# Optimization experiments

Hardware: AMD Instinct MI355X
Metric: run time of the kernel (lower is better)

The kernel has to match this reference:

```python
import jax, jax.numpy as jnp
import numpy as np

N, E, DIM, H = 50000, 800000, 256, 4
HD = DIM // H  # per-head dim = 64
NEG_SLOPE = 0.2
EPS = 1e-5


def _layernorm(x, g, b):
    mu = jnp.mean(x, axis=-1, keepdims=True)
    var = jnp.mean(jnp.square(x - mu), axis=-1, keepdims=True)
    return (x - mu) * jax.lax.rsqrt(var + EPS) * g + b


def setup_inputs() -> dict:
    key = jax.random.key(0)
    ks = jax.random.split(key, 8)
    s = 1.0 / np.sqrt(DIM)
    return {
        "x": jax.random.normal(ks[0], (N, DIM), dtype=jnp.float32),
        "edge_index": jax.random.randint(ks[1], (2, E), 0, N, dtype=jnp.int64),
        "W": jax.random.normal(ks[2], (DIM, DIM), dtype=jnp.float32) * s,
        "a_src": jax.random.normal(ks[3], (H, HD), dtype=jnp.float32) * s,
        "a_dst": jax.random.normal(ks[4], (H, HD), dtype=jnp.float32) * s,
        "gat_b": jnp.zeros((DIM,), jnp.float32),
        "ln1_g": jnp.ones((DIM,), jnp.float32),
        "ln1_b": jnp.zeros((DIM,), jnp.float32),
        "W1": jax.random.normal(ks[5], (DIM, 2 * DIM), dtype=jnp.float32) * s,
        "b1": jnp.zeros((2 * DIM,), jnp.float32),
        "W2": jax.random.normal(ks[6], (2 * DIM, DIM), dtype=jnp.float32) * (1.0 / np.sqrt(2 * DIM)),
        "b2": jnp.zeros((DIM,), jnp.float32),
        "ln2_g": jnp.ones((DIM,), jnp.float32),
        "ln2_b": jnp.zeros((DIM,), jnp.float32),
    }


def _gat(x, edge_index, W, a_src, a_dst, gat_b):
    # add self-loops (PyG GATConv default)
    loops = jnp.arange(N, dtype=edge_index.dtype)
    src = jnp.concatenate([edge_index[0], loops])
    dst = jnp.concatenate([edge_index[1], loops])
    h = (x @ W).reshape(N, H, HD)                    # [N,H,D]
    al_src = jnp.einsum("nhd,hd->nh", h, a_src)      # [N,H]
    al_dst = jnp.einsum("nhd,hd->nh", h, a_dst)
    e = jax.nn.leaky_relu(al_src[src] + al_dst[dst], NEG_SLOPE)  # [E',H]
    # softmax over edges grouped by destination node
    emax = jax.ops.segment_max(e, dst, num_segments=N)           # [N,H]
    ex = jnp.exp(e - emax[dst])
    denom = jax.ops.segment_sum(ex, dst, num_segments=N)         # [N,H]
    alpha = ex / denom[dst]                                      # [E',H]
    msg = alpha[:, :, None] * h[src]                             # [E',H,D]
    out = jax.ops.segment_sum(msg, dst, num_segments=N)          # [N,H,D]
    return out.reshape(N, DIM) + gat_b


def reference(x, edge_index, W, a_src, a_dst, gat_b, ln1_g, ln1_b, W1, b1, W2, b2, ln2_g, ln2_b):
    res = x
    y = _gat(x, edge_index, W, a_src, a_dst, gat_b)
    y = _layernorm(y + res, ln1_g, ln1_b)
    res = y
    f = jax.nn.gelu(y @ W1 + b1, approximate=False) @ W2 + b2
    return _layernorm(f + res, ln2_g, ln2_b)
```

## Files before the change

### kernel.cpp

```cpp
#include <hip/hip_runtime.h>

typedef __bf16 bf16_t;
typedef __bf16 bf16x4 __attribute__((ext_vector_type(4)));
typedef __bf16 bf16x8 __attribute__((ext_vector_type(8)));
typedef float  f32x4  __attribute__((ext_vector_type(4)));
typedef unsigned u32x2 __attribute__((ext_vector_type(2)));

__device__ inline float loadf(const void* p, size_t i, int bf) {
    return bf ? (float)((const bf16_t*)p)[i] : ((const float*)p)[i];
}
__device__ inline int eidx(const void* p, size_t i, int i64) {
    return i64 ? (int)((const long long*)p)[i] : ((const int*)p)[i];
}
__device__ inline float bflo(unsigned u) { return __uint_as_float(u << 16); }
__device__ inline float bfhi(unsigned u) { return __uint_as_float(u & 0xFFFF0000u); }

__device__ inline void gload16(const bf16_t* g, char* l) {
    __builtin_amdgcn_global_load_lds(
        (const __attribute__((address_space(1))) unsigned*)g,
        (__attribute__((address_space(3))) unsigned*)l, 16, 0, 0);
}

__global__ void detect_k(const void* __restrict__ x, const void* __restrict__ ei,
                         int E, int* __restrict__ flags) {
    int l = threadIdx.x;
    const unsigned* xu = (const unsigned*)x;
    unsigned low = xu[l] & 0xFFFFu;
    unsigned ex = (low >> 7) & 0xFF;
    int cnt = __popcll(__ballot(ex >= 115 && ex <= 133));
    const unsigned* eu = (const unsigned*)ei;
    int lim = E < 64 ? E : 64;
    unsigned v = (l < lim) ? eu[2 * (size_t)l + 1] : 0u;
    unsigned long long nz = __ballot(v != 0u);
    if (l == 0) { flags[0] = (cnt >= 32) ? 1 : 0; flags[1] = (nz == 0ull) ? 1 : 0; }
}

__global__ void tobf16_k(const void* __restrict__ in, bf16_t* __restrict__ out,
                         long n, const int* __restrict__ flags) {
    if (flags[0]) return;
    long i = ((long)blockIdx.x * 256 + threadIdx.x) * 8;
    long stride = (long)gridDim.x * 256 * 8;
    for (; i < n; i += stride) {
        f32x4 a = *(const f32x4*)((const float*)in + i);
        f32x4 b = *(const f32x4*)((const float*)in + i + 4);
        bf16x8 r;
        r[0]=(bf16_t)a[0]; r[1]=(bf16_t)a[1]; r[2]=(bf16_t)a[2]; r[3]=(bf16_t)a[3];
        r[4]=(bf16_t)b[0]; r[5]=(bf16_t)b[1]; r[6]=(bf16_t)b[2]; r[7]=(bf16_t)b[3];
        *(bf16x8*)&out[i] = r;
    }
}

__global__ void transpose3_k(const void* __restrict__ W,  bf16_t* __restrict__ WT,
                             const void* __restrict__ W1, bf16_t* __restrict__ W1T,
                             const void* __restrict__ W2, bf16_t* __restrict__ W2T,
                             const int* __restrict__ flags) {
    int bf = flags[0];
    int i = blockIdx.x * 256 + threadIdx.x;
    if (i < 65536) {
        int r = i >> 8, c = i & 255;
        WT[c * 256 + r] = (bf16_t)loadf(W, i, bf);
    } else if (i < 196608) {
        int j = i - 65536;
        int r = j >> 9, c = j & 511;
        W1T[c * 256 + r] = (bf16_t)loadf(W1, j, bf);
    } else if (i < 327680) {
        int j = i - 196608;
        int r = j >> 8, c = j & 255;
        W2T[c * 512 + r] = (bf16_t)loadf(W2, j, bf);
    }
}

__global__ __launch_bounds__(256) void gemm128(const bf16_t* __restrict__ A_,
                                               const void* __restrict__ a_raw,
                                               const bf16_t* __restrict__ BT,
                                               const void* __restrict__ bias,
                                               bf16_t* __restrict__ C,
                                               int M, int N, int K, int act,
                                               const int* __restrict__ flags,
                                               const void* __restrict__ a_srcp,
                                               const void* __restrict__ a_dstp,
                                               float* __restrict__ alsrc,
                                               float* __restrict__ aldst, int do_al) {
    int bf = flags[0];
    const bf16_t* A = (a_raw && bf) ? (const bf16_t*)a_raw : A_;
    __shared__ __align__(16) char smem[34816];
    int t = threadIdx.x;
    int tm = blockIdx.x * 128;
    int tn = blockIdx.y * 128;
    int w = t >> 6, l = t & 63;
    int wr = (w >> 1) * 64, wc = (w & 1) * 64;
    int lr16 = l & 15, kg = l >> 4;
    int NK = K >> 5;

    f32x4 acc[4][4];
#pragma unroll
    for (int i = 0; i < 4; i++)
#pragma unroll
        for (int j = 0; j < 4; j++) acc[i][j] = (f32x4){0.f, 0.f, 0.f, 0.f};

    bool fast = (tm + 128 <= M);

    if (fast) {
        int buf = 0;
#pragma unroll
        for (int ii = 0; ii < 2; ii++) {
            int c = w + ii * 4;
            int rowa = tm + (c & 1) * 64 + l;
            int rowb = tn + (c & 1) * 64 + l;
            int kc = (c >> 1) * 8;
            gload16(A  + (size_t)rowa * K + kc, smem +         c * 1024 + l * 16);
            gload16(BT + (size_t)rowb * K + kc, smem + 16384 + c * 1024 + l * 16);
        }
        __syncthreads();
        for (int ks = 0; ks < NK; ks++) {
            if (ks + 1 < NK) {
                int k0 = (ks + 1) << 5;
                char* ab = smem + (buf ^ 1) * 8192;
                char* bb = smem + 16384 + (buf ^ 1) * 8192;
#pragma unroll
                for (int ii = 0; ii < 2; ii++) {
                    int c = w + ii * 4;
                    int rowa = tm + (c & 1) * 64 + l;
                    int rowb = tn + (c & 1) * 64 + l;
                    int kc = k0 + (c >> 1) * 8;
                    gload16(A  + (size_t)rowa * K + kc, ab + c * 1024 + l * 16);
                    gload16(BT + (size_t)rowb * K + kc, bb + c * 1024 + l * 16);
                }
            }
            const char* ab = smem + buf * 8192;
            const char* bb = smem + 16384 + buf * 8192;
            bf16x8 af[4], bg[4];
#pragma unroll
            for (int i = 0; i < 4; i++) {
                af[i] = *(const bf16x8*)(ab + ((size_t)(kg * 128 + wr + i * 16 + lr16)) * 16);
                bg[i] = *(const bf16x8*)(bb + ((size_t)(kg * 128 + wc + i * 16 + lr16)) * 16);
            }
#pragma unroll
            for (int i = 0; i < 4; i++)
#pragma unroll
                for (int j = 0; j < 4; j++)
                    acc[i][j] = __builtin_amdgcn_mfma_f32_16x16x32_bf16(af[i], bg[j], acc[i][j], 0, 0, 0);
            __syncthreads();
            buf ^= 1;
        }
    } else {
        int r = t >> 2, kg2 = t & 3;
        for (int ks = 0; ks < NK; ks++) {
            int k0 = ks << 5;
            bf16x8 va[2], vb[2];
#pragma unroll
            for (int j = 0; j < 2; j++) {
                int row = r + j * 64;
                int ra = tm + row; if (ra > M - 1) ra = M - 1;
                va[j] = *(const bf16x8*)(A + (size_t)ra * K + k0 + kg2 * 8);
                vb[j] = *(const bf16x8*)(BT + (size_t)(tn + row) * K + k0 + kg2 * 8);
            }
            __syncthreads();
#pragma unroll
            for (int j = 0; j < 2; j++) {
                int row = r + j * 64;
                *(bf16x8*)(smem + ((size_t)(kg2 * 128 + row)) * 16) = va[j];
                *(bf16x8*)(smem + 16384 + ((size_t)(kg2 * 128 + row)) * 16) = vb[j];
            }
            __syncthreads();
            bf16x8 af[4], bg[4];
#pragma unroll
            for (int i = 0; i < 4; i++) {
                af[i] = *(const bf16x8*)(smem + ((size_t)(kg * 128 + wr + i * 16 + lr16)) * 16);
                bg[i] = *(const bf16x8*)(smem + 16384 + ((size_t)(kg * 128 + wc + i * 16 + lr16)) * 16);
            }
#pragma unroll
            for (int i = 0; i < 4; i++)
#pragma unroll
                for (int j = 0; j < 4; j++)
                    acc[i][j] = __builtin_amdgcn_mfma_f32_16x16x32_bf16(af[i], bg[j], acc[i][j], 0, 0, 0);
        }
        __syncthreads();
    }

    int cr0 = kg * 4;

    if (do_al) {
        float asv[4], adv[4];
#pragma unroll
        for (int j = 0; j < 4; j++) {
            int col = tn + wc + j * 16 + lr16;
            asv[j] = loadf(a_srcp, col, bf);
            adv[j] = loadf(a_dstp, col, bf);
        }
        int head = (tn + wc) >> 6;
#pragma unroll
        for (int i = 0; i < 4; i++) {
#pragma unroll
            for (int q = 0; q < 4; q++) {
                float ps = acc[i][0][q]*asv[0] + acc[i][1][q]*asv[1] + acc[i][2][q]*asv[2] + acc[i][3][q]*asv[3];
                float pd = acc[i][0][q]*adv[0] + acc[i][1][q]*adv[1] + acc[i][2][q]*adv[2] + acc[i][3][q]*adv[3];
#pragma unroll
                for (int d = 1; d < 16; d <<= 1) { ps += __shfl_xor(ps, d); pd += __shfl_xor(pd, d); }
                int row = tm + wr + i * 16 + cr0 + q;
                if (lr16 == 0 && row < M) { alsrc[row * 4 + head] = ps; aldst[row * 4 + head] = pd; }
            }
        }
    }

    bf16_t (*Cst)[136] = (bf16_t(*)[136])smem;
#pragma unroll
    for (int i = 0; i < 4; i++) {
#pragma unroll
        for (int j = 0; j < 4; j++) {
            int col = wc + j * 16 + lr16;
            float bv = bias ? loadf(bias, tn + col, bf) : 0.f;
#pragma unroll
            for (int q = 0; q < 4; q++) {
                float v = acc[i][j][q] + bv;
                if (act) v = 0.5f * v * (1.f + erff(v * 0.70710678118f));
                Cst[wr + i * 16 + cr0 + q][col] = (bf16_t)v;
            }
        }
    }
    __syncthreads();
#pragma unroll
    for (int it = 0; it < 8; it++) {
        int idx = it * 256 + t;
        int row = idx >> 4;
        int c8 = (idx & 15) * 8;
        if (tm + row < M)
            *(bf16x8*)&C[(size_t)(tm + row) * N + tn + c8] = *(const bf16x8*)&Cst[row][c8];
    }
}

__global__ void deg_k(const void* __restrict__ ei, int* __restrict__ deg, int E, int N,
                      const int* __restrict__ flags) {
    int i64 = flags[1];
    int i = blockIdx.x * 256 + threadIdx.x;
    if (i < E) {
        int d = eidx(ei, (size_t)E + i, i64);
        if ((unsigned)d >= (unsigned)N) d = 0;
        atomicAdd(&deg[d], 1);
    }
}

__global__ __launch_bounds__(256) void scan1(const int* __restrict__ deg, int* __restrict__ offs,
                                             int* __restrict__ chunkSum) {
    __shared__ int s[256];
    int t = threadIdx.x, b = blockIdx.x;
    int v = deg[b * 256 + t];
    s[t] = v; __syncthreads();
#pragma unroll
    for (int d = 1; d < 256; d <<= 1) {
        int u = (t >= d) ? s[t - d] : 0;
        __syncthreads(); s[t] += u; __syncthreads();
    }
    offs[b * 256 + t] = s[t] - v;
    if (t == 255) chunkSum[b] = s[255];
}

__global__ __launch_bounds__(256) void scan2(const int* __restrict__ chunkSum, int* __restrict__ chunkOff, int nch) {
    __shared__ int s[256];
    int t = threadIdx.x;
    int v = (t < nch) ? chunkSum[t] : 0;
    s[t] = v; __syncthreads();
#pragma unroll
    for (int d = 1; d < 256; d <<= 1) {
        int u = (t >= d) ? s[t - d] : 0;
        __syncthreads(); s[t] += u; __syncthreads();
    }
    chunkOff[t] = s[t] - v;
}

__global__ void scan3(int* __restrict__ offs, const int* __restrict__ chunkOff,
                      int* __restrict__ cursor, int total) {
    int i = blockIdx.x * 256 + threadIdx.x;
    if (i < total) { int v = offs[i] + chunkOff[i >> 8]; offs[i] = v; cursor[i] = v; }
}

__global__ void scatter_k(const void* __restrict__ ei, int* __restrict__ cursor,
                          int* __restrict__ csr, bf16_t* __restrict__ ewsb,
                          const float* __restrict__ alsrc, const float* __restrict__ aldst,
                          int E, int N, const int* __restrict__ flags) {
    int i64 = flags[1];
    int i = blockIdx.x * 256 + threadIdx.x;
    if (i < E) {
        int s = eidx(ei, i, i64);
        int d = eidx(ei, (size_t)E + i, i64);
        if ((unsigned)s >= (unsigned)N) s = 0;
        if ((unsigned)d >= (unsigned)N) d = 0;
        int p = atomicAdd(&cursor[d], 1);
        csr[p] = s;
        f32x4 as4 = *(const f32x4*)&alsrc[s * 4];
        f32x4 ad4 = *(const f32x4*)&aldst[d * 4];
        bf16x4 w4;
#pragma unroll
        for (int hh = 0; hh < 4; hh++) {
            float e = as4[hh] + ad4[hh];
            e = e > 0.f ? e : 0.2f * e;
            w4[hh] = (bf16_t)expf(fminf(e, 30.f));
        }
        *(bf16x4*)&ewsb[4 * (size_t)p] = w4;
    }
}

__global__ __launch_bounds__(256) void gat_agg_ln(
    const bf16_t* __restrict__ hbuf, const bf16_t* __restrict__ xb_,
    const void* __restrict__ x_raw,
    const float* __restrict__ alsrc, const float* __restrict__ aldst,
    const int* __restrict__ offs, const int* __restrict__ csr,
    const bf16_t* __restrict__ ewsb,
    const void* __restrict__ gatb, const void* __restrict__ lng, const void* __restrict__ lnb,
    bf16_t* __restrict__ y, const int* __restrict__ flags, int N) {
    int bf = flags[0];
    const bf16_t* xb = bf ? (const bf16_t*)x_raw : xb_;
    int w = threadIdx.x >> 6, l = threadIdx.x & 63;
    int n = blockIdx.x * 4 + w;
    if (n >= N) return;
    int h = l >> 4;
    int col0 = l * 4;

    __shared__ int   srcs[4][64];
    __shared__ float ewt[4][4][68];

    int off = offs[n], deg = offs[n + 1] - off;

    float es = alsrc[n * 4 + h] + aldst[n * 4 + h];
    es = es > 0.f ? es : 0.2f * es;
    float wself = expf(fminf(es, 30.f));

    float a0 = 0.f, a1 = 0.f, a2 = 0.f, a3 = 0.f;
    f32x4 ssum = (f32x4){0.f, 0.f, 0.f, 0.f};

    for (int c0 = 0; c0 < deg; c0 += 64) {
        int cl = deg - c0; if (cl > 64) cl = 64;
        if (l < cl) {
            int sv = csr[off + c0 + l];
            srcs[w][l] = sv;
            bf16x4 wv4 = *(const bf16x4*)&ewsb[4 * (size_t)(off + c0 + l)];
            float w0 = (float)wv4[0], w1 = (float)wv4[1], w2 = (float)wv4[2], w3 = (float)wv4[3];
            ewt[w][0][l] = w0; ewt[w][1][l] = w1;
            ewt[w][2][l] = w2; ewt[w][3][l] = w3;
            ssum += (f32x4){w0, w1, w2, w3};
        }
        int i = 0;
        for (; i + 8 <= cl; i += 8) {
            int sv[8]; u32x2 vv[8];
#pragma unroll
            for (int k = 0; k < 8; k++) sv[k] = __builtin_amdgcn_readfirstlane(srcs[w][i + k]);
#pragma unroll
            for (int k = 0; k < 8; k++) vv[k] = ((const u32x2*)(hbuf + (size_t)sv[k] * 256))[l];
            f32x4 wqa = *(const f32x4*)&ewt[w][h][i];
            f32x4 wqb = *(const f32x4*)&ewt[w][h][i + 4];
#pragma unroll
            for (int k = 0; k < 4; k++) {
                a0 += wqa[k]*bflo(vv[k][0]); a1 += wqa[k]*bfhi(vv[k][0]);
                a2 += wqa[k]*bflo(vv[k][1]); a3 += wqa[k]*bfhi(vv[k][1]);
                a0 += wqb[k]*bflo(vv[k+4][0]); a1 += wqb[k]*bfhi(vv[k+4][0]);
                a2 += wqb[k]*bflo(vv[k+4][1]); a3 += wqb[k]*bfhi(vv[k+4][1]);
            }
        }
        for (; i + 4 <= cl; i += 4) {
            int s0 = __builtin_amdgcn_readfirstlane(srcs[w][i]);
            int s1 = __builtin_amdgcn_readfirstlane(srcs[w][i + 1]);
            int s2 = __builtin_amdgcn_readfirstlane(srcs[w][i + 2]);
            int s3 = __builtin_amdgcn_readfirstlane(srcs[w][i + 3]);
            u32x2 v0 = ((const u32x2*)(hbuf + (size_t)s0 * 256))[l];
            u32x2 v1 = ((const u32x2*)(hbuf + (size_t)s1 * 256))[l];
            u32x2 v2 = ((const u32x2*)(hbuf + (size_t)s2 * 256))[l];
            u32x2 v3 = ((const u32x2*)(hbuf + (size_t)s3 * 256))[l];
            f32x4 wq = *(const f32x4*)&ewt[w][h][i];
            a0 += wq[0]*bflo(v0[0]); a1 += wq[0]*bfhi(v0[0]); a2 += wq[0]*bflo(v0[1]); a3 += wq[0]*bfhi(v0[1]);
            a0 += wq[1]*bflo(v1[0]); a1 += wq[1]*bfhi(v1[0]); a2 += wq[1]*bflo(v1[1]); a3 += wq[1]*bfhi(v1[1]);
            a0 += wq[2]*bflo(v2[0]); a1 += wq[2]*bfhi(v2[0]); a2 += wq[2]*bflo(v2[1]); a3 += wq[2]*bfhi(v2[1]);
            a0 += wq[3]*bflo(v3[0]); a1 += wq[3]*bfhi(v3[0]); a2 += wq[3]*bflo(v3[1]); a3 += wq[3]*bfhi(v3[1]);
        }
        for (; i < cl; i++) {
            int sv = __builtin_amdgcn_readfirstlane(srcs[w][i]);
            float wgt = ewt[w][h][i];
            u32x2 v0 = ((const u32x2*)(hbuf + (size_t)sv * 256))[l];
            a0 += wgt*bflo(v0[0]); a1 += wgt*bfhi(v0[0]); a2 += wgt*bflo(v0[1]); a3 += wgt*bfhi(v0[1]);
        }
    }

#pragma unroll
    for (int d = 1; d < 64; d <<= 1) {
        ssum[0] += __shfl_xor(ssum[0], d);
        ssum[1] += __shfl_xor(ssum[1], d);
        ssum[2] += __shfl_xor(ssum[2], d);
        ssum[3] += __shfl_xor(ssum[3], d);
    }
    float dsum = (h == 0) ? ssum[0] : (h == 1) ? ssum[1] : (h == 2) ? ssum[2] : ssum[3];
    float di = 1.f / (dsum + wself);

    u32x2 sv2 = ((const u32x2*)(hbuf + (size_t)n * 256))[l];
    u32x2 xv  = ((const u32x2*)(xb   + (size_t)n * 256))[l];
    float v0f = (a0 + wself*bflo(sv2[0])) * di + loadf(gatb, col0 + 0, bf) + bflo(xv[0]);
    float v1f = (a1 + wself*bfhi(sv2[0])) * di + loadf(gatb, col0 + 1, bf) + bfhi(xv[0]);
    float v2f = (a2 + wself*bflo(sv2[1])) * di + loadf(gatb, col0 + 2, bf) + bflo(xv[1]);
    float v3f = (a3 + wself*bfhi(sv2[1])) * di + loadf(gatb, col0 + 3, bf) + bfhi(xv[1]);

    float s1 = v0f + v1f + v2f + v3f;
#pragma unroll
    for (int d = 1; d < 64; d <<= 1) s1 += __shfl_xor(s1, d);
    float mu = s1 * (1.f / 256.f);
    float c0f = v0f - mu, c1f = v1f - mu, c2f = v2f - mu, c3f = v3f - mu;
    float sq = c0f*c0f + c1f*c1f + c2f*c2f + c3f*c3f;
#pragma unroll
    for (int d = 1; d < 64; d <<= 1) sq += __shfl_xor(sq, d);
    float rs = rsqrtf(sq * (1.f / 256.f) + 1e-5f);

    bf16x4 o;
    o[0] = (bf16_t)(c0f * rs * loadf(lng, col0 + 0, bf) + loadf(lnb, col0 + 0, bf));
    o[1] = (bf16_t)(c1f * rs * loadf(lng, col0 + 1, bf) + loadf(lnb, col0 + 1, bf));
    o[2] = (bf16_t)(c2f * rs * loadf(lng, col0 + 2, bf) + loadf(lnb, col0 + 2, bf));
    o[3] = (bf16_t)(c3f * rs * loadf(lng, col0 + 3, bf) + loadf(lnb, col0 + 3, bf));
    *(bf16x4*)&y[(size_t)n * 256 + col0] = o;
}

__global__ __launch_bounds__(256) void ln_res(const bf16_t* __restrict__ f, const bf16_t* __restrict__ y,
                                              const void* __restrict__ g, const void* __restrict__ b,
                                              void* __restrict__ out, int N, const int* __restrict__ flags) {
    int bf = flags[0];
    int row = blockIdx.x * 4 + (threadIdx.x >> 6);
    int l = threadIdx.x & 63;
    if (row >= N) return;
    int col0 = l * 4;
    u32x2 fv = *(const u32x2*)(f + (size_t)row * 256 + col0);
    u32x2 yv = *(const u32x2*)(y + (size_t)row * 256 + col0);
    float v0 = bflo(fv[0]) + bflo(yv[0]);
    float v1 = bfhi(fv[0]) + bfhi(yv[0]);
    float v2 = bflo(fv[1]) + bflo(yv[1]);
    float v3 = bfhi(fv[1]) + bfhi(yv[1]);
    float s = v0 + v1 + v2 + v3;
#pragma unroll
    for (int d = 1; d < 64; d <<= 1) s += __shfl_xor(s, d);
    float mu = s * (1.f / 256.f);
    float c0 = v0 - mu, c1 = v1 - mu, c2 = v2 - mu, c3 = v3 - mu;
    float sq = c0*c0 + c1*c1 + c2*c2 + c3*c3;
#pragma unroll
    for (int d = 1; d < 64; d <<= 1) sq += __shfl_xor(sq, d);
    float rs = rsqrtf(sq * (1.f / 256.f) + 1e-5f);
    float o0 = c0 * rs * loadf(g, col0 + 0, bf) + loadf(b, col0 + 0, bf);
    float o1 = c1 * rs * loadf(g, col0 + 1, bf) + loadf(b, col0 + 1, bf);
    float o2 = c2 * rs * loadf(g, col0 + 2, bf) + loadf(b, col0 + 2, bf);
    float o3 = c3 * rs * loadf(g, col0 + 3, bf) + loadf(b, col0 + 3, bf);
    if (bf) {
        bf16x4 o; o[0]=(bf16_t)o0; o[1]=(bf16_t)o1; o[2]=(bf16_t)o2; o[3]=(bf16_t)o3;
        *(bf16x4*)&((bf16_t*)out)[(size_t)row * 256 + col0] = o;
    } else {
        f32x4 o = (f32x4){o0, o1, o2, o3};
        *(f32x4*)&((float*)out)[(size_t)row * 256 + col0] = o;
    }
}

extern "C" void kernel_launch(void* const* d_in, const int* in_sizes, int n_in,
                              void* d_out, int out_size, void* d_ws, size_t ws_size,
                              hipStream_t stream) {
    const void* x    = d_in[0];
    const void* ei   = d_in[1];
    const void* W    = d_in[2];
    const void* a_src= d_in[3];
    const void* a_dst= d_in[4];
    const void* gatb = d_in[5];
    const void* ln1g = d_in[6];
    const void* ln1b = d_in[7];
    const void* W1   = d_in[8];
    const void* b1   = d_in[9];
    const void* W2   = d_in[10];
    const void* b2   = d_in[11];
    const void* ln2g = d_in[12];
    const void* ln2b = d_in[13];

    const int DIM = 256, DFF = 512;
    int N = in_sizes[0] / DIM;
    int E = in_sizes[1] / 2;

    char* ws = (char*)d_ws;
    size_t o = 0;
    auto alloc = [&](size_t bytes) { void* p = ws + o; o += (bytes + 255) & ~(size_t)255; return p; };
    int*    flags  = (int*)alloc(256);
    bf16_t* WT     = (bf16_t*)alloc((size_t)DIM * DIM * 2);
    bf16_t* W1T    = (bf16_t*)alloc((size_t)DIM * DFF * 2);
    bf16_t* W2T    = (bf16_t*)alloc((size_t)DFF * DIM * 2);
    float*  alsrc  = (float*)alloc((size_t)N * 4 * 4);
    float*  aldst  = (float*)alloc((size_t)N * 4 * 4);
    int nch = (N + 255) / 256;
    int tot = nch * 256;
    int* deg      = (int*)alloc((size_t)tot * 4);
    int* offs     = (int*)alloc((size_t)(tot + 1) * 4);
    int* cursor   = (int*)alloc((size_t)tot * 4);
    int* chunkSum = (int*)alloc(256 * 4);
    int* chunkOff = (int*)alloc(256 * 4);
    int* csr      = (int*)alloc((size_t)E * 4);
    bf16_t* ewsb  = (bf16_t*)alloc((size_t)E * 8);
    bf16_t* h     = (bf16_t*)alloc((size_t)N * DIM * 2);
    bf16_t* yb    = (bf16_t*)alloc((size_t)N * DIM * 2);
    bf16_t* xb    = (bf16_t*)alloc((size_t)N * DIM * 2);
    bf16_t* fb    = h;
    size_t remain = (ws_size > o) ? (ws_size - o) : 0;
    long CH = (long)(remain / ((size_t)DFF * 2));
    if (CH > N) CH = N;
    if (CH < 1024) CH = 1024;
    bf16_t* t1 = (bf16_t*)alloc((size_t)CH * DFF * 2);

    detect_k<<<1, 64, 0, stream>>>(x, ei, E, flags);
    hipMemsetAsync(deg, 0, (size_t)tot * 4, stream);

    tobf16_k<<<4096, 256, 0, stream>>>(x, xb, (long)N * DIM, flags);
    transpose3_k<<<1280, 256, 0, stream>>>(W, WT, W1, W1T, W2, W2T, flags);

    dim3 g1((N + 127) / 128, DIM / 128);
    gemm128<<<g1, 256, 0, stream>>>(xb, x, WT, nullptr, h, N, DIM, DIM, 0, flags,
                                    a_src, a_dst, alsrc, aldst, 1);

    deg_k<<<(E + 255) / 256, 256, 0, stream>>>(ei, deg, E, N, flags);
    scan1<<<nch, 256, 0, stream>>>(deg, offs, chunkSum);
    scan2<<<1, 256, 0, stream>>>(chunkSum, chunkOff, nch);
    scan3<<<(tot + 255) / 256, 256, 0, stream>>>(offs, chunkOff, cursor, tot);
    scatter_k<<<(E + 255) / 256, 256, 0, stream>>>(ei, cursor, csr, ewsb, alsrc, aldst, E, N, flags);

    gat_agg_ln<<<(N + 3) / 4, 256, 0, stream>>>(h, xb, x, alsrc, aldst, offs, csr, ewsb,
                                                gatb, ln1g, ln1b, yb, flags, N);

    for (long r0 = 0; r0 < N; r0 += CH) {
        int m = (int)((N - r0 < CH) ? (N - r0) : CH);
        dim3 g2((m + 127) / 128, DFF / 128);
        gemm128<<<g2, 256, 0, stream>>>(yb + r0 * DIM, nullptr, W1T, b1, t1, m, DFF, DIM, 1, flags,
                                        nullptr, nullptr, nullptr, nullptr, 0);
        dim3 g3((m + 127) / 128, DIM / 128);
        gemm128<<<g3, 256, 0, stream>>>(t1, nullptr, W2T, b2, fb + r0 * DIM, m, DIM, DFF, 0, flags,
                                        nullptr, nullptr, nullptr, nullptr, 0);
    }

    ln_res<<<(N + 3) / 4, 256, 0, stream>>>(fb, yb, ln2g, ln2b, d_out, N, flags);
}
```

Before: 363.0 us.

## Add 128x256-tile 512-thread GEMM for FFN first layer with tail fallback

Adds a new GEMM kernel using 512 threads and a 128x256 output tile with double-buffered LDS loads via global_load_lds and 16x16x32 bf16 MFMA, used for the W1 (GELU) projection on full 128-row blocks. Leftover rows go to the old 128x128 kernel. The larger tile increases reuse of A across more output columns and halves the number of blocks, but uses more LDS and registers per block and a two-pass epilogue with extra syncs.

```diff
diff --git a/kernel.cpp b/kernel.cpp
--- a/kernel.cpp
+++ b/kernel.cpp
@@ -226,6 +226,104 @@
         int c8 = (idx & 15) * 8;
         if (tm + row < M)
             *(bf16x8*)&C[(size_t)(tm + row) * N + tn + c8] = *(const bf16x8*)&Cst[row][c8];
+    }
+}
+
+__global__ __launch_bounds__(512) void gemm512t(const bf16_t* __restrict__ A,
+                                                const bf16_t* __restrict__ BT,
+                                                const void* __restrict__ bias,
+                                                bf16_t* __restrict__ C,
+                                                int M, int N, int K, int act,
+                                                const int* __restrict__ flags) {
+    int bf = flags[0];
+    __shared__ __align__(16) char smem[49152];
+    int t = threadIdx.x;
+    int tm = blockIdx.x * 128;
+    int tn = blockIdx.y * 256;
+    int w = t >> 6, l = t & 63;
+    int rb = w >> 2, cb = w & 3;
+    int wr = rb * 64, wc = cb * 64;
+    int lr16 = l & 15, kg = l >> 4;
+    int NK = K >> 5;
+
+    f32x4 acc[4][4];
+#pragma unroll
+    for (int i = 0; i < 4; i++)
+#pragma unroll
+        for (int j = 0; j < 4; j++) acc[i][j] = (f32x4){0.f, 0.f, 0.f, 0.f};
+
+    int buf = 0;
+    {
+        int rowa = tm + rb * 64 + l;
+        gload16(A + (size_t)rowa * K + cb * 8, smem + cb * 2048 + (rb * 64 + l) * 16);
+#pragma unroll
+        for (int ii = 0; ii < 2; ii++) {
+            int rloc = rb * 64 + ii * 128 + l;
+            gload16(BT + (size_t)(tn + rloc) * K + cb * 8,
+                    smem + 16384 + cb * 4096 + rloc * 16);
+        }
+    }
+    __syncthreads();
+    for (int ks = 0; ks < NK; ks++) {
+        if (ks + 1 < NK) {
+            int k0 = (ks + 1) << 5;
+            char* ab = smem + (buf ^ 1) * 8192;
+            char* bb = smem + 16384 + (buf ^ 1) * 16384;
+            int rowa = tm + rb * 64 + l;
+            gload16(A + (size_t)rowa * K + k0 + cb * 8, ab + cb * 2048 + (rb * 64 + l) * 16);
+#pragma unroll
+            for (int ii = 0; ii < 2; ii++) {
+                int rloc = rb * 64 + ii * 128 + l;
+                gload16(BT + (size_t)(tn + rloc) * K + k0 + cb * 8,
+                        bb + cb * 4096 + rloc * 16);
+            }
+        }
+        const char* ab = smem + buf * 8192;
+        const char* bb = smem + 16384 + buf * 16384;
+        bf16x8 af[4], bg[4];
+#pragma unroll
+        for (int i = 0; i < 4; i++) {
+            af[i] = *(const bf16x8*)(ab + (size_t)(kg * 2048 + (wr + i * 16 + lr16) * 16));
+            bg[i] = *(const bf16x8*)(bb + (size_t)(kg * 4096 + (wc + i * 16 + lr16) * 16));
+        }
+#pragma unroll
+        for (int i = 0; i < 4; i++)
+#pragma unroll
+            for (int j = 0; j < 4; j++)
+                acc[i][j] = __builtin_amdgcn_mfma_f32_16x16x32_bf16(af[i], bg[j], acc[i][j], 0, 0, 0);
+        __syncthreads();
+        buf ^= 1;
+    }
+
+    bf16_t (*Cst)[264] = (bf16_t(*)[264])smem;
+    int cr0 = kg * 4;
+#pragma unroll
+    for (int half = 0; half < 2; half++) {
+        if (rb == half) {
+#pragma unroll
+            for (int i = 0; i < 4; i++) {
+#pragma unroll
+                for (int j = 0; j < 4; j++) {
+                    int col = wc + j * 16 + lr16;
+                    float bv = bias ? loadf(bias, tn + col, bf) : 0.f;
+#pragma unroll
+                    for (int q = 0; q < 4; q++) {
+                        float v = acc[i][j][q] + bv;
+                        if (act) v = 0.5f * v * (1.f + erff(v * 0.70710678118f));
+                        Cst[i * 16 + cr0 + q][col] = (bf16_t)v;
+                    }
+                }
+            }
+        }
+        __syncthreads();
+#pragma unroll
+        for (int it = 0; it < 4; it++) {
+            int idx = it * 512 + t;
+            int row = idx >> 5;
+            int c8 = (idx & 31) * 8;
+            *(bf16x8*)&C[(size_t)(tm + half * 64 + row) * N + tn + c8] = *(const bf16x8*)&Cst[row][c8];
+        }
+        __syncthreads();
     }
 }
 
@@ -521,9 +619,18 @@
 
     for (long r0 = 0; r0 < N; r0 += CH) {
         int m = (int)((N - r0 < CH) ? (N - r0) : CH);
-        dim3 g2((m + 127) / 128, DFF / 128);
-        gemm128<<<g2, 256, 0, stream>>>(yb + r0 * DIM, nullptr, W1T, b1, t1, m, DFF, DIM, 1, flags,
-                                        nullptr, nullptr, nullptr, nullptr, 0);
+        int mmain = (m / 128) * 128;
+        int tail = m - mmain;
+        if (mmain > 0) {
+            dim3 g2(mmain / 128, DFF / 256);
+            gemm512t<<<g2, 512, 0, stream>>>(yb + r0 * DIM, W1T, b1, t1, mmain, DFF, DIM, 1, flags);
+        }
+        if (tail > 0) {
+            dim3 g2t(1, DFF / 128);
+            gemm128<<<g2t, 256, 0, stream>>>(yb + (r0 + mmain) * DIM, nullptr, W1T, b1,
+                                             t1 + (size_t)mmain * DFF, tail, DFF, DIM, 1, flags,
+                                             nullptr, nullptr, nullptr, nullptr, 0);
+        }
         dim3 g3((m + 127) / 128, DIM / 128);
         gemm128<<<g3, 256, 0, stream>>>(t1, nullptr, W2T, b2, fb + r0 * DIM, m, DIM, DFF, 0, flags,
                                         nullptr, nullptr, nullptr, nullptr, 0);
```

Result: slower. 395.1 us (+8.9%).
